# Kernel tuning notes

Hardware: AMD Instinct MI355X
Metric: run time of the kernel (lower is better)

The kernel has to match this reference:

```python
import jax, jax.numpy as jnp
import numpy as np

N = 50000      # nodes
E = 800000     # edges (before self-loops)
G = 500        # graphs
IN = 128       # in_channels
HID = 32       # hidden_channels per head
HEADS = 4
C = HID * HEADS        # 128, per-layer output dim
L = 3                  # num_layers
HL = (L * C) // 2      # 192, JK-LSTM hidden size (PyG convention)
OUT = 2
NEG_SLOPE = 0.2


def setup_inputs() -> dict:
    key = jax.random.key(0)
    ks = iter(jax.random.split(key, 40))
    inp = {}
    inp['x'] = jax.random.normal(next(ks), (N, IN), dtype=jnp.float32)
    inp['edge_index'] = jax.random.randint(next(ks), (2, E), 0, N, dtype=jnp.int32)
    inp['batch'] = jnp.sort(jax.random.randint(next(ks), (N,), 0, G, dtype=jnp.int32))
    s = 0.1
    for i, in_dim in enumerate([IN, C, C]):
        inp[f'W{i}'] = jax.random.normal(next(ks), (in_dim, C), dtype=jnp.float32) * s
        inp[f'as{i}'] = jax.random.normal(next(ks), (HEADS, HID), dtype=jnp.float32) * s
        inp[f'ad{i}'] = jax.random.normal(next(ks), (HEADS, HID), dtype=jnp.float32) * s
        inp[f'b{i}'] = jnp.zeros((C,), dtype=jnp.float32)
    for d in ['f', 'b']:
        inp[f'Wih_{d}'] = jax.random.normal(next(ks), (4 * HL, C), dtype=jnp.float32) * s
        inp[f'Whh_{d}'] = jax.random.normal(next(ks), (4 * HL, HL), dtype=jnp.float32) * s
        inp[f'bih_{d}'] = jnp.zeros((4 * HL,), dtype=jnp.float32)
        inp[f'bhh_{d}'] = jnp.zeros((4 * HL,), dtype=jnp.float32)
    inp['Wa'] = jax.random.normal(next(ks), (2 * HL, 1), dtype=jnp.float32) * s
    inp['ba'] = jnp.zeros((1,), dtype=jnp.float32)
    inp['Wl'] = jax.random.normal(next(ks), (C, OUT), dtype=jnp.float32) * s
    inp['bl'] = jnp.zeros((OUT,), dtype=jnp.float32)
    return inp


def gat_conv(h_in, src, dst, W, a_s, a_d, b, n):
    # h: [n, heads, hid]
    h = (h_in @ W).reshape(n, HEADS, HID)
    es = (h * a_s).sum(-1)   # [n, heads]
    ed = (h * a_d).sum(-1)
    e = jax.nn.leaky_relu(es[src] + ed[dst], NEG_SLOPE)  # [e, heads]
    m = jax.ops.segment_max(e, dst, num_segments=n)
    ex = jnp.exp(e - m[dst])
    ssum = jax.ops.segment_sum(ex, dst, num_segments=n)
    alpha = ex / (ssum[dst] + 1e-16)
    out = jax.ops.segment_sum(h[src] * alpha[:, :, None], dst, num_segments=n)
    return out.reshape(n, HEADS * HID) + b


def lstm_dir(xseq, Wih, Whh, bih, bhh):
    # xseq: [L, n, C] -> hs: [L, n, HL]; torch gate order i,f,g,o
    n = xseq.shape[1]
    h0 = jnp.zeros((n, HL), xseq.dtype)

    def step(carry, xt):
        h, c = carry
        z = xt @ Wih.T + h @ Whh.T + bih + bhh
        i, f, g, o = jnp.split(z, 4, axis=-1)
        c = jax.nn.sigmoid(f) * c + jax.nn.sigmoid(i) * jnp.tanh(g)
        h = jax.nn.sigmoid(o) * jnp.tanh(c)
        return (h, c), h

    _, hs = jax.lax.scan(step, (h0, h0), xseq)
    return hs


def reference(x, edge_index, batch, W0, as0, ad0, b0, W1, as1, ad1, b1,
              W2, as2, ad2, b2, Wih_f, Whh_f, bih_f, bhh_f,
              Wih_b, Whh_b, bih_b, bhh_b, Wa, ba, Wl, bl):
    n = x.shape[0]
    loop = jnp.arange(n, dtype=edge_index.dtype)
    src = jnp.concatenate([edge_index[0], loop])  # add_self_loops=True
    dst = jnp.concatenate([edge_index[1], loop])
    h = x
    xs = []
    for (W, a_s, a_d, b) in [(W0, as0, ad0, b0), (W1, as1, ad1, b1), (W2, as2, ad2, b2)]:
        h = jax.nn.relu(gat_conv(h, src, dst, W, a_s, a_d, b, n))
        xs.append(h)  # dropout is identity in eval mode
    xstack = jnp.stack(xs, axis=1)  # [n, L, C]
    xseq = jnp.stack(xs, axis=0)    # [L, n, C]
    hs_f = lstm_dir(xseq, Wih_f, Whh_f, bih_f, bhh_f)
    hs_b = lstm_dir(xseq[::-1], Wih_b, Whh_b, bih_b, bhh_b)[::-1]
    lo = jnp.concatenate([hs_f, hs_b], axis=-1)       # [L, n, 2*HL]
    score = jnp.einsum('lnh,h->nl', lo, Wa[:, 0]) + ba[0]
    att = jax.nn.softmax(score, axis=-1)              # [n, L]
    jk = jnp.einsum('nlc,nl->nc', xstack, att)        # [n, C]
    ones = jnp.ones((n,), x.dtype)
    counts = jax.ops.segment_sum(ones, batch, num_segments=G)
    pooled = jax.ops.segment_sum(jk, batch, num_segments=G) / jnp.maximum(counts, 1.0)[:, None]
    return pooled @ Wl + bl  # [G, OUT]
```

## Files before the change

kernel.cpp:

```cpp
#include <hip/hip_runtime.h>
#include <math.h>

#define CDIV(a,b) (((a)+(b)-1)/(b))

typedef _Float16 f16;
typedef _Float16 f16x8 __attribute__((ext_vector_type(8)));
typedef float f32x4 __attribute__((ext_vector_type(4)));

__device__ __forceinline__ float rcpf(float x){ return __builtin_amdgcn_rcpf(x); }
__device__ __forceinline__ float fsig(float x){ return rcpf(1.0f+__expf(-x)); }
__device__ __forceinline__ float ftanh(float x){ float e=__expf(2.0f*x); return 1.0f-2.0f*rcpf(e+1.0f); }

__global__ void zero_kernel(float* __restrict__ p, size_t n){
  size_t i=(size_t)blockIdx.x*blockDim.x+threadIdx.x;
  size_t st=(size_t)gridDim.x*blockDim.x;
  for(;i<n;i+=st) p[i]=0.0f;
}

__global__ void f2h_kernel(const float* __restrict__ s, f16* __restrict__ d, size_t n){
  size_t i=(size_t)blockIdx.x*blockDim.x+threadIdx.x;
  size_t st=(size_t)gridDim.x*blockDim.x;
  for(;i<n;i+=st) d[i]=(f16)s[i];
}
__global__ void wtrans_kernel(const float* __restrict__ W, f16* __restrict__ hi,
                              f16* __restrict__ lo){
  int o=blockIdx.x, i=threadIdx.x;
  float f=W[(size_t)i*128+o];
  f16 h=(f16)f; hi[o*128+i]=h; lo[o*128+i]=(f16)(f-(float)h);
}
__global__ void lstm_wprep(const float* __restrict__ W, f16* __restrict__ hi, int ld){
  int rn=blockIdx.x; int k=threadIdx.x;
  int j=rn>>2, gate=rn&3;
  hi[(size_t)rn*ld+k]=(f16)W[(size_t)(gate*192+j)*ld + k];
}
__global__ void lstm_bprep(const float* __restrict__ bih, const float* __restrict__ bhh,
                           float* __restrict__ bI){
  int rn=blockIdx.x*blockDim.x+threadIdx.x;
  if(rn<768){ int j=rn>>2,g=rn&3; int go=g*192+j; bI[rn]=bih[go]+bhh[go]; }
}

__global__ void hist_kernel(const int* __restrict__ ei, int E, int N, int* __restrict__ deg){
  int e=blockIdx.x*blockDim.x+threadIdx.x;
  if(e>=E+N) return;
  int d=(e<E)? ei[E+e] : (e-E);
  atomicAdd(&deg[d],1);
}
__global__ void scan1_kernel(const int* __restrict__ deg, int* __restrict__ offs,
                             int* __restrict__ bsums, int N){
  __shared__ int sd[1024];
  int t=threadIdx.x;
  int i=blockIdx.x*1024+t;
  int v=(i<N)?deg[i]:0;
  sd[t]=v;
  __syncthreads();
  for(int s=1;s<1024;s<<=1){
    int u=(t>=s)?sd[t-s]:0;
    __syncthreads();
    sd[t]+=u;
    __syncthreads();
  }
  if(i<N) offs[i]=sd[t]-v;
  if(t==1023) bsums[blockIdx.x]=sd[1023];
}
__global__ void scan2_kernel(int* __restrict__ bsums, int* __restrict__ offs, int NB, int N){
  if(threadIdx.x==0&&blockIdx.x==0){
    int run=0;
    for(int b=0;b<NB;b++){int s=bsums[b]; bsums[b]=run; run+=s;}
    offs[N]=run;
  }
}
__global__ void scan3_kernel(int* __restrict__ offs, const int* __restrict__ bsums,
                             int* __restrict__ cursor, int N){
  int i=blockIdx.x*blockDim.x+threadIdx.x;
  if(i<N){
    int o=offs[i]+bsums[i>>10];
    offs[i]=o;
    cursor[i]=o;
  }
}
__global__ void scatter_kernel(const int* __restrict__ ei, int E, int N,
                               int* __restrict__ cursor, int* __restrict__ csr){
  int e=blockIdx.x*blockDim.x+threadIdx.x;
  if(e>=E+N) return;
  int s,d;
  if(e<E){ s=ei[e]; d=ei[E+e]; } else { s=e-E; d=s; }
  int pos=atomicAdd(&cursor[d],1);
  csr[pos]=s;
}

__global__ void goffs_kernel(const int* __restrict__ batch, int N, int G,
                             int* __restrict__ goffs){
  int g=blockIdx.x*blockDim.x+threadIdx.x;
  if (g>G) return;
  if (g==G){ goffs[G]=N; return; }
  int lo=0, hi=N;
  while (lo<hi){ int mid=(lo+hi)>>1; if (batch[mid]<g) lo=mid+1; else hi=mid; }
  goffs[g]=lo;
}

struct GemmDesc {
  const f16* aq[2][12];
  const f16* bq[2][12];
  int lda[12], ldb[12];
  int nq, nd, M, GY, NXB;
  f16* htmp; const float* as_; const float* ad_; float* es; float* ed;
  f16* h16[2]; f16* cbuf[2]; const float* bias[2]; const float* wa[2];
  float* score; int l_out[2]; int firstStep; int lastStep;
};

template<int MODE>
__global__ __launch_bounds__(256) void gemm_mfma(GemmDesc d){
  __shared__ __align__(16) char smraw[33792];
  const int TILE = 128*32;
  f16* Ab0=(f16*)smraw;      f16* Ab1=Ab0+TILE;
  f16* Bb0=Ab1+TILE;         f16* Bb1=Bb0+TILE;
  float* EP = (float*)smraw;

  const int wg = blockIdx.x;
  const int xcd = wg & 7, kk0 = wg >> 3;
  const int nxt = d.nd * d.NXB;
  const int xbg = kk0 % nxt;
  const int yp  = xcd + 8*(kk0 / nxt);
  if (yp >= d.GY) return;
  const int dir = (xbg >= d.NXB) ? 1 : 0;
  const int xb  = xbg - dir*d.NXB;

  const int t = threadIdx.x;
  const int wv = t>>6, ln = t&63;
  const int m0 = yp*128, n0 = xb*128;
  const int wr = (wv>>1)*64, wc = (wv&1)*64;
  f32x4 acc[4][4];
#pragma unroll
  for(int i=0;i<4;i++)
#pragma unroll
  for(int j=0;j<4;j++) acc[i][j]=(f32x4){0.f,0.f,0.f,0.f};

  const int gs = ((ln&3) - ((ln>>3)&3)) & 3;
  const int gp = ((ln>>4) + (((ln&15)>>1)&3)) & 3;

  int offA128[2],offA192[2],offB128[2],offB192[2];
#pragma unroll
  for(int i=0;i<2;i++){
    int ga = m0 + i*64 + wv*16 + (ln>>2); if (ga >= d.M) ga = d.M-1;
    int gb = n0 + i*64 + wv*16 + (ln>>2);
    offA128[i]=ga*128+gs*8; offA192[i]=ga*192+gs*8;
    offB128[i]=gb*128+gs*8; offB192[i]=gb*192+gs*8;
  }

  auto issue=[&](int q,int buf){
    const f16* aS=d.aq[dir][q]; const bool wa_=(d.lda[q]==192);
    const f16* bS=d.bq[dir][q]; const bool wb_=(d.ldb[q]==192);
    f16* Adst = buf? Ab1:Ab0;
    f16* Bdst = buf? Bb1:Bb0;
#pragma unroll
    for(int i=0;i<2;i++){
      int offa = wa_? offA192[i]:offA128[i];
      __builtin_amdgcn_global_load_lds(
        (const __attribute__((address_space(1))) unsigned int*)(aS+offa),
        (__attribute__((address_space(3))) unsigned int*)&Adst[(i*64+wv*16)*32],16,0,0);
      int offb = wb_? offB192[i]:offB128[i];
      __builtin_amdgcn_global_load_lds(
        (const __attribute__((address_space(1))) unsigned int*)(bS+offb),
        (__attribute__((address_space(3))) unsigned int*)&Bdst[(i*64+wv*16)*32],16,0,0);
    }
  };

  issue(0,0);
  for (int s=0; s<d.nq; s++){
    const int cur = s&1;
    if (s+1<d.nq){
      issue(s+1,cur^1);
      asm volatile("s_waitcnt vmcnt(4)" ::: "memory");
    } else {
      asm volatile("s_waitcnt vmcnt(0)" ::: "memory");
    }
    __builtin_amdgcn_sched_barrier(0);
    __builtin_amdgcn_s_barrier();
    __builtin_amdgcn_sched_barrier(0);
    const f16* As = cur? Ab1:Ab0;
    const f16* Bs = cur? Bb1:Bb0;
    f16x8 av[4], bv[4];
#pragma unroll
    for (int i=0;i<4;i++)
      av[i] = *(const f16x8*)&As[(wr + i*16 + (ln&15))*32 + gp*8];
#pragma unroll
    for (int j=0;j<4;j++)
      bv[j] = *(const f16x8*)&Bs[(wc + j*16 + (ln&15))*32 + gp*8];
#pragma unroll
    for (int i=0;i<4;i++)
#pragma unroll
    for (int j=0;j<4;j++)
      acc[i][j] = __builtin_amdgcn_mfma_f32_16x16x32_f16(av[i], bv[j], acc[i][j], 0,0,0);
    __builtin_amdgcn_sched_barrier(0);
    __builtin_amdgcn_s_barrier();
  }

  const int lc2 = ln&15, lr4 = (ln>>4)*4;
  const int row4 = t>>2, q4 = t&3;
#pragma unroll
  for (int ph=0; ph<2; ph++){
    __syncthreads();
    if ((wv>>1) == ph){
#pragma unroll
      for (int i=0;i<4;i++){
#pragma unroll
        for (int jf=0;jf<4;jf++){
          int col = wc + jf*16 + lc2;
#pragma unroll
          for (int r=0;r<4;r++)
            EP[(i*16+lr4+r)*132 + col] = acc[i][jf][r];
        }
      }
    }
    __syncthreads();
    int grow = m0 + ph*64 + row4;
    if (grow < d.M){
      if (MODE==0){
        float s=0.f, dd=0.f;
        const float* asp = d.as_ + q4*32;
        const float* adp = d.ad_ + q4*32;
#pragma unroll
        for (int q8=0;q8<4;q8++){
          f16x8 pk;
#pragma unroll
          for (int r=0;r<8;r++){
            float v = EP[row4*132 + q4*32 + q8*8 + r];
            pk[r] = (f16)v;
            s  += v*asp[q8*8+r];
            dd += v*adp[q8*8+r];
          }
          *(f16x8*)&d.htmp[(size_t)grow*128 + q4*32 + q8*8] = pk;
        }
        d.es[grow*4+q4] = s;
        d.ed[grow*4+q4] = dd;
      } else {
        float sc = 0.f;
        int jg0 = xb*32 + q4*8;
        size_t hbase = (size_t)grow*192 + jg0;
        const float* bI = d.bias[dir] + xb*128 + q4*32;
        f16* h16d = d.h16[dir];
        f16* cbufd = d.cbuf[dir];
        const float* wad = d.wa[dir];
        f16x8 cold8;
        if (!d.firstStep) cold8 = *(const f16x8*)&cbufd[hbase];
        f16x8 hl, cl;
#pragma unroll
        for (int j=0;j<8;j++){
          float4 z = *(float4*)&EP[row4*132 + q4*32 + j*4];
          float zi=z.x+bI[j*4+0], zf=z.y+bI[j*4+1], zg=z.z+bI[j*4+2], zo=z.w+bI[j*4+3];
          float cold = d.firstStep ? 0.f : (float)cold8[j];
          float c = fsig(zf)*cold + fsig(zi)*ftanh(zg);
          float h = fsig(zo)*ftanh(c);
          cl[j] = (f16)c;
          hl[j] = (f16)h;
          sc += h * wad[jg0+j];
        }
        if (!d.lastStep){
          *(f16x8*)&cbufd[hbase] = cl;
          *(f16x8*)&h16d[hbase] = hl;
        }
        sc += __shfl_xor(sc,1);
        sc += __shfl_xor(sc,2);
        if (q4==0) atomicAdd(&d.score[(size_t)grow*3 + d.l_out[dir]], sc);
      }
    }
  }
}

__global__ __launch_bounds__(256) void attn_kernel(const f16* __restrict__ htmp,
   const float* __restrict__ es, const float* __restrict__ ed,
   const int* __restrict__ offs, const int* __restrict__ csr,
   const float* __restrict__ bias, f16* __restrict__ xsl, int N){
  int v=blockIdx.x*4+(threadIdx.x>>6);
  if(v>=N) return;
  int lane=threadIdx.x&63;
  int hd=lane>>4;
  int c0=lane*2;
  int beg=offs[v], end=offs[v+1];
  float edv=ed[v*4+hd];
  float ssum=0.f,a0=0.f,a1=0.f;
  int i=beg;
  for(; i+8<=end; i+=8){
    int sv[8];
#pragma unroll
    for(int k=0;k<8;k++) sv[k]=csr[i+k];
    float Ev[8]; unsigned uv[8];
#pragma unroll
    for(int k=0;k<8;k++){
      Ev[k]=es[sv[k]*4+hd];
      uv[k]=*(const unsigned*)&htmp[(size_t)sv[k]*128+c0];
    }
#pragma unroll
    for(int k=0;k<8;k++){
      float e=Ev[k]+edv; e=(e>0.f)?e:0.2f*e;
      float x=__expf(e);
      ssum+=x;
      union {unsigned u; f16 h[2];} pk; pk.u=uv[k];
      a0+=x*(float)pk.h[0]; a1+=x*(float)pk.h[1];
    }
  }
  for(; i+4<=end; i+=4){
    int s0=csr[i],s1=csr[i+1],s2=csr[i+2],s3=csr[i+3];
    float E0=es[s0*4+hd],E1=es[s1*4+hd],E2=es[s2*4+hd],E3=es[s3*4+hd];
    unsigned u0=*(const unsigned*)&htmp[(size_t)s0*128+c0];
    unsigned u1=*(const unsigned*)&htmp[(size_t)s1*128+c0];
    unsigned u2=*(const unsigned*)&htmp[(size_t)s2*128+c0];
    unsigned u3=*(const unsigned*)&htmp[(size_t)s3*128+c0];
    float e0=E0+edv; e0=(e0>0.f)?e0:0.2f*e0; float x0=__expf(e0);
    float e1=E1+edv; e1=(e1>0.f)?e1:0.2f*e1; float x1=__expf(e1);
    float e2=E2+edv; e2=(e2>0.f)?e2:0.2f*e2; float x2=__expf(e2);
    float e3=E3+edv; e3=(e3>0.f)?e3:0.2f*e3; float x3=__expf(e3);
    ssum += (x0+x1)+(x2+x3);
    union {unsigned u; f16 h[2];} p0,p1,p2,p3;
    p0.u=u0; p1.u=u1; p2.u=u2; p3.u=u3;
    a0 += x0*(float)p0.h[0] + x1*(float)p1.h[0] + x2*(float)p2.h[0] + x3*(float)p3.h[0];
    a1 += x0*(float)p0.h[1] + x1*(float)p1.h[1] + x2*(float)p2.h[1] + x3*(float)p3.h[1];
  }
  for(; i<end; i++){
    int s=csr[i];
    float e=es[s*4+hd]+edv;
    e=(e>0.f)?e:0.2f*e;
    float ex=__expf(e);
    ssum+=ex;
    union {unsigned u; f16 h[2];} pk;
    pk.u = *reinterpret_cast<const unsigned*>(&htmp[(size_t)s*128+c0]);
    a0+=ex*(float)pk.h[0]; a1+=ex*(float)pk.h[1];
  }
  float inv=1.0f/(ssum+1e-16f);
  float o0=fmaxf(a0*inv+bias[c0],0.f), o1=fmaxf(a1*inv+bias[c0+1],0.f);
  union { f16 h[2]; unsigned u; } pko;
  pko.h[0]=(f16)o0; pko.h[1]=(f16)o1;
  *reinterpret_cast<unsigned*>(&xsl[(size_t)v*128+c0]) = pko.u;
}

__global__ __launch_bounds__(256) void jk_pool_kernel(const f16* __restrict__ xs, size_t xstride,
   const float* __restrict__ score, const int* __restrict__ goffs,
   float* __restrict__ pooled, int G){
  int g=blockIdx.x;
  int beg=goffs[g], end=goffs[g+1];
  int c=threadIdx.x&127, half=threadIdx.x>>7;
  float acc=0.f;
  for(int n=beg+half; n<end; n+=2){
    float s0=score[n*3],s1=score[n*3+1],s2=score[n*3+2];
    float m=fmaxf(s0,fmaxf(s1,s2));
    float e0=__expf(s0-m),e1=__expf(s1-m),e2=__expf(s2-m);
    float inv=rcpf(e0+e1+e2);
    size_t base=(size_t)n*128+c;
    acc += ((float)xs[base]*e0+(float)xs[xstride+base]*e1+(float)xs[2*xstride+base]*e2)*inv;
  }
  __shared__ float red[128];
  if(half==1) red[c]=acc;
  __syncthreads();
  if(half==0){
    float tot=acc+red[c];
    float cnt=(float)(end-beg);
    pooled[(size_t)g*128+c]=tot*rcpf(fmaxf(cnt,1.0f));
  }
}

__global__ __launch_bounds__(128) void final_kernel(const float* __restrict__ pooled,
   const float* __restrict__ Wl, const float* __restrict__ bl,
   float* __restrict__ out, int G){
  int g=blockIdx.x; int c=threadIdx.x;
  float pv=pooled[(size_t)g*128+c];
  float p0=pv*Wl[c*2], p1=pv*Wl[c*2+1];
  for(int s=32;s>=1;s>>=1){ p0+=__shfl_down(p0,s); p1+=__shfl_down(p1,s); }
  __shared__ float sm[4];
  int w=c>>6;
  if((c&63)==0){ sm[w*2]=p0; sm[w*2+1]=p1; }
  __syncthreads();
  if(c==0){
    out[g*2+0]=sm[0]+sm[2]+bl[0];
    out[g*2+1]=sm[1]+sm[3]+bl[1];
  }
}

extern "C" void kernel_launch(void* const* d_in, const int* in_sizes, int n_in,
                              void* d_out, int out_size, void* d_ws, size_t ws_size,
                              hipStream_t stream) {
  const float* x     = (const float*)d_in[0];
  const int*   ei    = (const int*)d_in[1];
  const int*   batch = (const int*)d_in[2];
  const float* W[3]  = {(const float*)d_in[3],(const float*)d_in[7],(const float*)d_in[11]};
  const float* AS[3] = {(const float*)d_in[4],(const float*)d_in[8],(const float*)d_in[12]};
  const float* AD[3] = {(const float*)d_in[5],(const float*)d_in[9],(const float*)d_in[13]};
  const float* BV[3] = {(const float*)d_in[6],(const float*)d_in[10],(const float*)d_in[14]};
  const float* Wih[2]= {(const float*)d_in[15],(const float*)d_in[19]};
  const float* Whh[2]= {(const float*)d_in[16],(const float*)d_in[20]};
  const float* bih[2]= {(const float*)d_in[17],(const float*)d_in[21]};
  const float* bhh[2]= {(const float*)d_in[18],(const float*)d_in[22]};
  const float* Wa    = (const float*)d_in[23];
  const float* Wl    = (const float*)d_in[25];
  const float* bl    = (const float*)d_in[26];
  float* out = (float*)d_out;

  const int N  = in_sizes[2];
  const int E  = in_sizes[1]/2;
  const int ET = E+N;
  const int G  = out_size/2;
  const int Mpad = CDIV(N,128)*128;
  const int GY = CDIV(N,128);
  const int GYp = CDIV(GY,8)*8;

  char* p = (char*)d_ws;
  auto alloc = [&](size_t bytes)->char*{ char* r=p; p += ((bytes+255)/256)*256; return r; };
  int*   deg    = (int*)  alloc((size_t)N*4);
  int*   offs   = (int*)  alloc((size_t)(N+1)*4);
  int*   cursor = (int*)  alloc((size_t)N*4);
  int*   bsums  = (int*)  alloc((size_t)CDIV(N,1024)*4);
  int*   csr    = (int*)  alloc((size_t)ET*4);
  int*   goffs  = (int*)  alloc((size_t)(G+1)*4);
  f16*   WtH[3], *WtL[3];
  for(int l=0;l<3;l++){ WtH[l]=(f16*)alloc(128*128*2); WtL[l]=(f16*)alloc(128*128*2); }
  f16 *WihH[2],*WhhH[2];
  float* bsumI[2];
  for(int d2=0;d2<2;d2++){
    WihH[d2]=(f16*)alloc(768*128*2);
    WhhH[d2]=(f16*)alloc(768*192*2);
    bsumI[d2]=(float*)alloc(768*4);
  }
  f16*   xs16   = (f16*)  alloc((size_t)3*Mpad*128*2);
  float* score  = (float*)alloc((size_t)N*3*4);
  float* pooled = (float*)alloc((size_t)G*128*4);
  char* P = p;
  auto al256 = [](size_t b)->size_t{ return ((b+255)/256)*256; };
  f16*   x016 = (f16*)P;
  f16*   htmp = (f16*)(P + al256((size_t)Mpad*128*2));
  float* esb  = (float*)((char*)htmp + al256((size_t)Mpad*128*2));
  float* edb  = (float*)((char*)esb + al256((size_t)N*4*4));
  f16*  h16s[2]; f16* cbufs[2];
  {
    char* q = P;
    h16s[0]=(f16*)q;   q += al256((size_t)Mpad*192*2);
    cbufs[0]=(f16*)q;  q += al256((size_t)Mpad*192*2);
    h16s[1]=(f16*)q;   q += al256((size_t)Mpad*192*2);
    cbufs[1]=(f16*)q;
  }

  const size_t xstride = (size_t)Mpad*128;

  f2h_kernel<<<512,256,0,stream>>>(x, x016, (size_t)N*128);
  for(int l=0;l<3;l++) wtrans_kernel<<<128,128,0,stream>>>(W[l], WtH[l], WtL[l]);
  for(int d2=0;d2<2;d2++){
    lstm_wprep<<<768,128,0,stream>>>(Wih[d2], WihH[d2], 128);
    lstm_wprep<<<768,192,0,stream>>>(Whh[d2], WhhH[d2], 192);
    lstm_bprep<<<3,256,0,stream>>>(bih[d2], bhh[d2], bsumI[d2]);
  }
  zero_kernel<<<64,256,0,stream>>>(score,(size_t)N*3);
  goffs_kernel<<<CDIV(G+1,256),256,0,stream>>>(batch,N,G,goffs);

  zero_kernel<<<64,256,0,stream>>>((float*)deg,(size_t)N);
  hist_kernel<<<CDIV(ET,256),256,0,stream>>>(ei,E,N,deg);
  int NB = CDIV(N,1024);
  scan1_kernel<<<NB,1024,0,stream>>>(deg,offs,bsums,N);
  scan2_kernel<<<1,64,0,stream>>>(bsums,offs,NB,N);
  scan3_kernel<<<CDIV(N,256),256,0,stream>>>(offs,bsums,cursor,N);
  scatter_kernel<<<CDIV(ET,256),256,0,stream>>>(ei,E,N,cursor,csr);

  const f16* ain = x016;
  for (int l=0; l<3; l++){
    GemmDesc gd{};
    gd.nq=8; gd.nd=1; gd.M=N; gd.GY=GY; gd.NXB=1;
    gd.htmp=htmp; gd.as_=AS[l]; gd.ad_=AD[l]; gd.es=esb; gd.ed=edb;
    for(int qq=0;qq<4;qq++){
      gd.aq[0][2*qq+0]=ain+qq*32;  gd.bq[0][2*qq+0]=WtH[l]+qq*32;
      gd.aq[0][2*qq+1]=ain+qq*32;  gd.bq[0][2*qq+1]=WtL[l]+qq*32;
    }
    for(int qq=0;qq<8;qq++){ gd.lda[qq]=128; gd.ldb[qq]=128; }
    gemm_mfma<0><<<GYp,256,0,stream>>>(gd);
    attn_kernel<<<CDIV(N,4),256,0,stream>>>(htmp,esb,edb,offs,csr,BV[l],
                                            xs16+(size_t)l*xstride,N);
    ain = xs16+(size_t)l*xstride;
  }

  for (int st=0; st<3; st++){
    GemmDesc gd{};
    gd.nd=2; gd.NXB=6; gd.M=N; gd.GY=GY;
    gd.nq = (st==0)?4:10;
    gd.score=score; gd.firstStep=(st==0); gd.lastStep=(st==2);
    for(int dir2=0;dir2<2;dir2++){
      int l_in = dir2? (2-st):st;
      gd.l_out[dir2]=l_in;
      const f16* xt = xs16 + (size_t)l_in*xstride;
      gd.h16[dir2]=h16s[dir2]; gd.cbuf[dir2]=cbufs[dir2];
      gd.bias[dir2]=bsumI[dir2]; gd.wa[dir2]=Wa+dir2*192;
      for(int qq=0;qq<4;qq++){
        gd.aq[dir2][qq]=xt+qq*32;
        gd.bq[dir2][qq]=WihH[dir2]+qq*32;
      }
      for(int qq=4;qq<10;qq++){
        gd.aq[dir2][qq]=h16s[dir2]+(qq-4)*32;
        gd.bq[dir2][qq]=WhhH[dir2]+(qq-4)*32;
      }
    }
    for(int qq=0;qq<4;qq++){ gd.lda[qq]=128; gd.ldb[qq]=128; }
    for(int qq=4;qq<10;qq++){ gd.lda[qq]=192; gd.ldb[qq]=192; }
    gemm_mfma<1><<<12*GYp,256,0,stream>>>(gd);
  }

  jk_pool_kernel<<<G,256,0,stream>>>(xs16,xstride,score,goffs,pooled,G);
  final_kernel<<<G,128,0,stream>>>(pooled,Wl,bl,out,G);
}
```

Before: 600.4 us.

## Split LSTM GEMM into dedicated kernel with 128x256 tiles

Separates the templated GEMM into a GAT-specific kernel and an LSTM-specific kernel. The LSTM kernel widens the N tile from 128 to 256 (each wave computes 64x128 with 4x8 MFMA accumulators), halving the number of workgroups and the redundant reloads of the A operand (x and h) across output column blocks. It raises shared memory to 48KB and doubles the accumulator registers per thread, which can reduce occupancy, and the epilogue now runs in four phases.

```diff
diff --git a/kernel.cpp b/kernel.cpp
--- a/kernel.cpp
+++ b/kernel.cpp
@@ -98,18 +98,13 @@
   goffs[g]=lo;
 }
 
-struct GemmDesc {
-  const f16* aq[2][12];
-  const f16* bq[2][12];
-  int lda[12], ldb[12];
-  int nq, nd, M, GY, NXB;
+struct GatDesc {
+  const f16* aq[12]; const f16* bq[12];
+  int nq, M, GY;
   f16* htmp; const float* as_; const float* ad_; float* es; float* ed;
-  f16* h16[2]; f16* cbuf[2]; const float* bias[2]; const float* wa[2];
-  float* score; int l_out[2]; int firstStep; int lastStep;
 };
 
-template<int MODE>
-__global__ __launch_bounds__(256) void gemm_mfma(GemmDesc d){
+__global__ __launch_bounds__(256) void gemm_gat(GatDesc d){
   __shared__ __align__(16) char smraw[33792];
   const int TILE = 128*32;
   f16* Ab0=(f16*)smraw;      f16* Ab1=Ab0+TILE;
@@ -118,16 +113,12 @@
 
   const int wg = blockIdx.x;
   const int xcd = wg & 7, kk0 = wg >> 3;
-  const int nxt = d.nd * d.NXB;
-  const int xbg = kk0 % nxt;
-  const int yp  = xcd + 8*(kk0 / nxt);
+  const int yp  = xcd + 8*kk0;
   if (yp >= d.GY) return;
-  const int dir = (xbg >= d.NXB) ? 1 : 0;
-  const int xb  = xbg - dir*d.NXB;
 
   const int t = threadIdx.x;
   const int wv = t>>6, ln = t&63;
-  const int m0 = yp*128, n0 = xb*128;
+  const int m0 = yp*128;
   const int wr = (wv>>1)*64, wc = (wv&1)*64;
   f32x4 acc[4][4];
 #pragma unroll
@@ -138,29 +129,25 @@
   const int gs = ((ln&3) - ((ln>>3)&3)) & 3;
   const int gp = ((ln>>4) + (((ln&15)>>1)&3)) & 3;
 
-  int offA128[2],offA192[2],offB128[2],offB192[2];
+  int offA[2],offB[2];
 #pragma unroll
   for(int i=0;i<2;i++){
     int ga = m0 + i*64 + wv*16 + (ln>>2); if (ga >= d.M) ga = d.M-1;
-    int gb = n0 + i*64 + wv*16 + (ln>>2);
-    offA128[i]=ga*128+gs*8; offA192[i]=ga*192+gs*8;
-    offB128[i]=gb*128+gs*8; offB192[i]=gb*192+gs*8;
+    int gb = i*64 + wv*16 + (ln>>2);
+    offA[i]=ga*128+gs*8; offB[i]=gb*128+gs*8;
   }
 
   auto issue=[&](int q,int buf){
-    const f16* aS=d.aq[dir][q]; const bool wa_=(d.lda[q]==192);
-    const f16* bS=d.bq[dir][q]; const bool wb_=(d.ldb[q]==192);
+    const f16* aS=d.aq[q]; const f16* bS=d.bq[q];
     f16* Adst = buf? Ab1:Ab0;
     f16* Bdst = buf? Bb1:Bb0;
 #pragma unroll
     for(int i=0;i<2;i++){
-      int offa = wa_? offA192[i]:offA128[i];
       __builtin_amdgcn_global_load_lds(
-        (const __attribute__((address_space(1))) unsigned int*)(aS+offa),
+        (const __attribute__((address_space(1))) unsigned int*)(aS+offA[i]),
         (__attribute__((address_space(3))) unsigned int*)&Adst[(i*64+wv*16)*32],16,0,0);
-      int offb = wb_? offB192[i]:offB128[i];
       __builtin_amdgcn_global_load_lds(
-        (const __attribute__((address_space(1))) unsigned int*)(bS+offb),
+        (const __attribute__((address_space(1))) unsigned int*)(bS+offB[i]),
         (__attribute__((address_space(3))) unsigned int*)&Bdst[(i*64+wv*16)*32],16,0,0);
     }
   };
@@ -215,54 +202,176 @@
     __syncthreads();
     int grow = m0 + ph*64 + row4;
     if (grow < d.M){
-      if (MODE==0){
-        float s=0.f, dd=0.f;
-        const float* asp = d.as_ + q4*32;
-        const float* adp = d.ad_ + q4*32;
-#pragma unroll
-        for (int q8=0;q8<4;q8++){
-          f16x8 pk;
-#pragma unroll
-          for (int r=0;r<8;r++){
-            float v = EP[row4*132 + q4*32 + q8*8 + r];
-            pk[r] = (f16)v;
-            s  += v*asp[q8*8+r];
-            dd += v*adp[q8*8+r];
-          }
-          *(f16x8*)&d.htmp[(size_t)grow*128 + q4*32 + q8*8] = pk;
+      float s=0.f, dd=0.f;
+      const float* asp = d.as_ + q4*32;
+      const float* adp = d.ad_ + q4*32;
+#pragma unroll
+      for (int q8=0;q8<4;q8++){
+        f16x8 pk;
+#pragma unroll
+        for (int r=0;r<8;r++){
+          float v = EP[row4*132 + q4*32 + q8*8 + r];
+          pk[r] = (f16)v;
+          s  += v*asp[q8*8+r];
+          dd += v*adp[q8*8+r];
         }
-        d.es[grow*4+q4] = s;
-        d.ed[grow*4+q4] = dd;
-      } else {
-        float sc = 0.f;
-        int jg0 = xb*32 + q4*8;
-        size_t hbase = (size_t)grow*192 + jg0;
-        const float* bI = d.bias[dir] + xb*128 + q4*32;
-        f16* h16d = d.h16[dir];
-        f16* cbufd = d.cbuf[dir];
-        const float* wad = d.wa[dir];
-        f16x8 cold8;
-        if (!d.firstStep) cold8 = *(const f16x8*)&cbufd[hbase];
-        f16x8 hl, cl;
-#pragma unroll
-        for (int j=0;j<8;j++){
-          float4 z = *(float4*)&EP[row4*132 + q4*32 + j*4];
-          float zi=z.x+bI[j*4+0], zf=z.y+bI[j*4+1], zg=z.z+bI[j*4+2], zo=z.w+bI[j*4+3];
-          float cold = d.firstStep ? 0.f : (float)cold8[j];
-          float c = fsig(zf)*cold + fsig(zi)*ftanh(zg);
-          float h = fsig(zo)*ftanh(c);
-          cl[j] = (f16)c;
-          hl[j] = (f16)h;
-          sc += h * wad[jg0+j];
+        *(f16x8*)&d.htmp[(size_t)grow*128 + q4*32 + q8*8] = pk;
+      }
+      d.es[grow*4+q4] = s;
+      d.ed[grow*4+q4] = dd;
+    }
+  }
+}
+
+struct LstmDesc {
+  const f16* aq[2][10]; const f16* bq[2][10];
+  int lda[10], ldb[10];
+  int nq, M, GY;
+  f16* h16[2]; f16* cbuf[2]; const float* bias[2]; const float* wa[2];
+  float* score; int l_out[2]; int firstStep; int lastStep;
+};
+
+__global__ __launch_bounds__(256) void gemm_lstm(LstmDesc d){
+  __shared__ __align__(16) char smraw[49152];
+  const int AT = 128*32, BT = 256*32;
+  f16* As0=(f16*)smraw;  f16* As1=As0+AT;
+  f16* Bs0=As1+AT;       f16* Bs1=Bs0+BT;
+  float* EP=(float*)smraw;
+
+  const int wg = blockIdx.x;
+  const int xcd = wg & 7, kk0 = wg >> 3;
+  const int xbg = kk0 % 6;
+  const int yp  = xcd + 8*(kk0 / 6);
+  if (yp >= d.GY) return;
+  const int dir = (xbg >= 3) ? 1 : 0;
+  const int xb  = xbg - dir*3;
+
+  const int t = threadIdx.x;
+  const int wv = t>>6, ln = t&63;
+  const int m0 = yp*128, n0 = xb*256;
+  const int wr = (wv>>1)*64, wc = (wv&1)*128;
+  f32x4 acc[4][8];
+#pragma unroll
+  for(int i=0;i<4;i++)
+#pragma unroll
+  for(int j=0;j<8;j++) acc[i][j]=(f32x4){0.f,0.f,0.f,0.f};
+
+  const int gs = ((ln&3) - ((ln>>3)&3)) & 3;
+  const int gp = ((ln>>4) + (((ln&15)>>1)&3)) & 3;
+
+  int offA128[2],offA192[2],offB128[4],offB192[4];
+#pragma unroll
+  for(int i=0;i<2;i++){
+    int ga = m0 + i*64 + wv*16 + (ln>>2); if (ga >= d.M) ga = d.M-1;
+    offA128[i]=ga*128+gs*8; offA192[i]=ga*192+gs*8;
+  }
+#pragma unroll
+  for(int k=0;k<4;k++){
+    int gb = n0 + k*64 + wv*16 + (ln>>2);
+    offB128[k]=gb*128+gs*8; offB192[k]=gb*192+gs*8;
+  }
+
+  auto issue=[&](int q,int buf){
+    const f16* aS=d.aq[dir][q]; const bool wa_=(d.lda[q]==192);
+    const f16* bS=d.bq[dir][q]; const bool wb_=(d.ldb[q]==192);
+    f16* Adst = buf? As1:As0;
+    f16* Bdst = buf? Bs1:Bs0;
+#pragma unroll
+    for(int i=0;i<2;i++){
+      int offa = wa_? offA192[i]:offA128[i];
+      __builtin_amdgcn_global_load_lds(
+        (const __attribute__((address_space(1))) unsigned int*)(aS+offa),
+        (__attribute__((address_space(3))) unsigned int*)&Adst[(i*64+wv*16)*32],16,0,0);
+    }
+#pragma unroll
+    for(int k=0;k<4;k++){
+      int offb = wb_? offB192[k]:offB128[k];
+      __builtin_amdgcn_global_load_lds(
+        (const __attribute__((address_space(1))) unsigned int*)(bS+offb),
+        (__attribute__((address_space(3))) unsigned int*)&Bdst[(k*64+wv*16)*32],16,0,0);
+    }
+  };
+
+  issue(0,0);
+  for (int s=0; s<d.nq; s++){
+    const int cur = s&1;
+    if (s+1<d.nq){
+      issue(s+1,cur^1);
+      asm volatile("s_waitcnt vmcnt(6)" ::: "memory");
+    } else {
+      asm volatile("s_waitcnt vmcnt(0)" ::: "memory");
+    }
+    __builtin_amdgcn_sched_barrier(0);
+    __builtin_amdgcn_s_barrier();
+    __builtin_amdgcn_sched_barrier(0);
+    const f16* As = cur? As1:As0;
+    const f16* Bs = cur? Bs1:Bs0;
+    f16x8 av[4], bv[8];
+#pragma unroll
+    for (int i=0;i<4;i++)
+      av[i] = *(const f16x8*)&As[(wr + i*16 + (ln&15))*32 + gp*8];
+#pragma unroll
+    for (int j=0;j<8;j++)
+      bv[j] = *(const f16x8*)&Bs[(wc + j*16 + (ln&15))*32 + gp*8];
+#pragma unroll
+    for (int i=0;i<4;i++)
+#pragma unroll
+    for (int j=0;j<8;j++)
+      acc[i][j] = __builtin_amdgcn_mfma_f32_16x16x32_f16(av[i], bv[j], acc[i][j], 0,0,0);
+    __builtin_amdgcn_sched_barrier(0);
+    __builtin_amdgcn_s_barrier();
+  }
+
+  const int lc2 = ln&15, lr4 = (ln>>4)*4;
+  const int row4 = t>>3, q8 = t&7;
+#pragma unroll
+  for (int ph=0; ph<4; ph++){
+    __syncthreads();
+    if ((wv>>1) == (ph>>1)){
+#pragma unroll
+      for (int i2=0;i2<2;i2++){
+        int i = (ph&1)*2 + i2;
+#pragma unroll
+        for (int jf=0;jf<8;jf++){
+          int col = wc + jf*16 + lc2;
+#pragma unroll
+          for (int r=0;r<4;r++)
+            EP[(i2*16+lr4+r)*264 + col] = acc[i][jf][r];
         }
-        if (!d.lastStep){
-          *(f16x8*)&cbufd[hbase] = cl;
-          *(f16x8*)&h16d[hbase] = hl;
-        }
-        sc += __shfl_xor(sc,1);
-        sc += __shfl_xor(sc,2);
-        if (q4==0) atomicAdd(&d.score[(size_t)grow*3 + d.l_out[dir]], sc);
       }
+    }
+    __syncthreads();
+    int grow = m0 + ph*32 + row4;
+    if (grow < d.M){
+      float sc = 0.f;
+      int jg0 = xb*64 + q8*8;
+      size_t hbase = (size_t)grow*192 + jg0;
+      const float* bI = d.bias[dir] + xb*256 + q8*32;
+      f16* h16d = d.h16[dir];
+      f16* cbufd = d.cbuf[dir];
+      const float* wad = d.wa[dir];
+      f16x8 cold8;
+      if (!d.firstStep) cold8 = *(const f16x8*)&cbufd[hbase];
+      f16x8 hl, cl;
+#pragma unroll
+      for (int j=0;j<8;j++){
+        float4 z = *(float4*)&EP[row4*264 + q8*32 + j*4];
+        float zi=z.x+bI[j*4+0], zf=z.y+bI[j*4+1], zg=z.z+bI[j*4+2], zo=z.w+bI[j*4+3];
+        float cold = d.firstStep ? 0.f : (float)cold8[j];
+        float c = fsig(zf)*cold + fsig(zi)*ftanh(zg);
+        float h = fsig(zo)*ftanh(c);
+        cl[j] = (f16)c;
+        hl[j] = (f16)h;
+        sc += h * wad[jg0+j];
+      }
+      if (!d.lastStep){
+        *(f16x8*)&cbufd[hbase] = cl;
+        *(f16x8*)&h16d[hbase] = hl;
+      }
+      sc += __shfl_xor(sc,1);
+      sc += __shfl_xor(sc,2);
+      sc += __shfl_xor(sc,4);
+      if ((t&7)==0) atomicAdd(&d.score[(size_t)grow*3 + d.l_out[dir]], sc);
     }
   }
 }
@@ -459,23 +568,22 @@
 
   const f16* ain = x016;
   for (int l=0; l<3; l++){
-    GemmDesc gd{};
-    gd.nq=8; gd.nd=1; gd.M=N; gd.GY=GY; gd.NXB=1;
+    GatDesc gd{};
+    gd.nq=8; gd.M=N; gd.GY=GY;
     gd.htmp=htmp; gd.as_=AS[l]; gd.ad_=AD[l]; gd.es=esb; gd.ed=edb;
     for(int qq=0;qq<4;qq++){
-      gd.aq[0][2*qq+0]=ain+qq*32;  gd.bq[0][2*qq+0]=WtH[l]+qq*32;
-      gd.aq[0][2*qq+1]=ain+qq*32;  gd.bq[0][2*qq+1]=WtL[l]+qq*32;
-    }
-    for(int qq=0;qq<8;qq++){ gd.lda[qq]=128; gd.ldb[qq]=128; }
-    gemm_mfma<0><<<GYp,256,0,stream>>>(gd);
+      gd.aq[2*qq+0]=ain+qq*32;  gd.bq[2*qq+0]=WtH[l]+qq*32;
+      gd.aq[2*qq+1]=ain+qq*32;  gd.bq[2*qq+1]=WtL[l]+qq*32;
+    }
+    gemm_gat<<<GYp,256,0,stream>>>(gd);
     attn_kernel<<<CDIV(N,4),256,0,stream>>>(htmp,esb,edb,offs,csr,BV[l],
                                             xs16+(size_t)l*xstride,N);
     ain = xs16+(size_t)l*xstride;
   }
 
   for (int st=0; st<3; st++){
-    GemmDesc gd{};
-    gd.nd=2; gd.NXB=6; gd.M=N; gd.GY=GY;
+    LstmDesc gd{};
+    gd.M=N; gd.GY=GY;
     gd.nq = (st==0)?4:10;
     gd.score=score; gd.firstStep=(st==0); gd.lastStep=(st==2);
     for(int dir2=0;dir2<2;dir2++){
@@ -495,7 +603,7 @@
     }
     for(int qq=0;qq<4;qq++){ gd.lda[qq]=128; gd.ldb[qq]=128; }
     for(int qq=4;qq<10;qq++){ gd.lda[qq]=192; gd.ldb[qq]=192; }
-    gemm_mfma<1><<<12*GYp,256,0,stream>>>(gd);
+    gemm_lstm<<<6*GYp,256,0,stream>>>(gd);
   }
 
   jk_pool_kernel<<<G,256,0,stream>>>(xs16,xstride,score,goffs,pooled,G);
```

New measurement: 623.3 us. 1.04x slower.
